# Performance work log

Measured on AMD Instinct MI355X. Metric: run time of the kernel, lower is better.

## Reference

```python
import jax, jax.numpy as jnp
import numpy as np

N, K, B, C, H = 12000, 32, 1, 64, 64
ALPHA = 0.3  # keras LeakyReLU default

def leaky(x):
    return jnp.where(x >= 0, x, ALPHA * x)

def setup_inputs() -> dict:
    key = jax.random.key(0)
    ks = jax.random.split(key, 8)
    def dense_init(k, fan_in, fan_out):
        lim = np.sqrt(6.0 / (fan_in + fan_out))
        return jax.random.uniform(k, (fan_in, fan_out), jnp.float32, -lim, lim)
    return {
        "embeddings": jax.random.normal(ks[0], (B, N, C), jnp.float32),
        "weights": jax.random.uniform(ks[1], (N, N), jnp.float32),
        "neighbor_set": jax.random.randint(ks[2], (N, K), 0, N, jnp.int64) if jax.config.jax_enable_x64 else jax.random.randint(ks[2], (N, K), 0, N, jnp.int32),
        "Q0_w": dense_init(ks[3], C, H), "Q0_b": jnp.zeros((H,), jnp.float32),
        "W0_w": dense_init(ks[4], C + H, H), "W0_b": jnp.zeros((H,), jnp.float32),
        "Q1_w": dense_init(ks[5], H, H), "Q1_b": jnp.zeros((H,), jnp.float32),
        "W1_w": dense_init(ks[6], H + H, H), "W1_b": jnp.zeros((H,), jnp.float32),
    }

def convolve(emb, weights, nbr, Qw, Qb, Ww, Wb):
    # emb: [B,N,C], weights: [N,N], nbr: [N,K]
    nb_emb = emb[:, nbr, :]                       # [B,N,K,C] gather neighbors
    nb_hid = leaky(jnp.einsum('bnkc,ch->bnkh', nb_emb, Qw) + Qb)  # [B,N,K,H]
    nb_w = weights[jnp.arange(nbr.shape[0])[:, None], nbr]        # [N,K]
    nb_w = nb_w[None, :, :, None]                                  # [1,N,K,1]
    agg = jnp.sum(nb_hid * nb_w, axis=2) / (jnp.sum(nb_w, axis=2) + 1e-6)  # [B,N,H]
    cat = jnp.concatenate([emb, agg], axis=-1)     # [B,N,C+H]
    out = leaky(jnp.einsum('bnd,dh->bnh', cat, Ww) + Wb)
    return out / (jnp.linalg.norm(out, axis=2, keepdims=True) + 1e-6)

def reference(embeddings, weights, neighbor_set, Q0_w, Q0_b, W0_w, W0_b, Q1_w, Q1_b, W1_w, W1_b):
    x = convolve(embeddings, weights, neighbor_set, Q0_w, Q0_b, W0_w, W0_b)
    x = convolve(x, weights, neighbor_set, Q1_w, Q1_b, W1_w, W1_b)
    return x
```

## Files before the change

kernel.cpp:

```cpp
#include <hip/hip_runtime.h>
#include <math.h>

#define ALPHA 0.3f
#define KN 32

__device__ __forceinline__ float leaky_f(float x) { return x >= 0.f ? x : ALPHA * x; }

__global__ __launch_bounds__(256) void k_dense_gather(
    const float* __restrict__ X,
    const float* __restrict__ Qw,
    const float* __restrict__ Qb,
    const float* __restrict__ wmat,
    const int*  __restrict__ nbr,
    float* __restrict__ wcache,
    float* __restrict__ Hout,
    int N)
{
    __shared__ float sQ[64 * 64];
    __shared__ float sX[4][64];
    const int tid  = threadIdx.x;
    const int wid  = tid >> 6;
    const int lane = tid & 63;
    const int bs   = blockIdx.x * 16;

    int gid[2]; float gw[2];
    #pragma unroll
    for (int u = 0; u < 2; ++u) {
        int e = tid + u * 256;
        int n = bs + (e >> 5); if (n >= N) n = N - 1;
        gid[u] = nbr[(size_t)n * KN + (e & 31)];
    }
    #pragma unroll
    for (int u = 0; u < 2; ++u) {
        int e = tid + u * 256;
        int n = bs + (e >> 5); if (n >= N) n = N - 1;
        gw[u] = wmat[(size_t)n * (size_t)N + gid[u]];
    }

    {
        const float4* s = (const float4*)Qw; float4* d = (float4*)sQ;
        #pragma unroll
        for (int i = 0; i < 4; ++i) d[i * 256 + tid] = s[i * 256 + tid];
    }
    __syncthreads();

    const float qb = Qb[lane];
    #pragma unroll
    for (int g = 0; g < 4; ++g) {
        int nr = bs + g * 4 + wid;
        int n  = nr < N ? nr : N - 1;
        sX[wid][lane] = X[(size_t)n * 64 + lane];
        float acc = qb;
        #pragma unroll
        for (int c = 0; c < 64; ++c)
            acc = fmaf(sX[wid][c], sQ[c * 64 + lane], acc);
        if (nr < N) Hout[(size_t)n * 64 + lane] = leaky_f(acc);
    }

    if (wcache) {
        #pragma unroll
        for (int u = 0; u < 2; ++u) {
            int e = tid + u * 256;
            if (bs + (e >> 5) < N) wcache[(size_t)bs * KN + e] = gw[u];
        }
    }
}

template<bool FUSE>
__global__ __launch_bounds__(256) void k_conv(
    const float* __restrict__ X,
    const float* __restrict__ Hbuf,
    const float* __restrict__ Wmat,
    const float* __restrict__ wcache,
    const int*  __restrict__ nbr,
    const float* __restrict__ Ww,
    const float* __restrict__ Wb,
    const float* __restrict__ Q1w,
    const float* __restrict__ Q1b,
    float* __restrict__ OUT,
    float* __restrict__ H1out,
    int N, int mode)
{
    __shared__ float sW[128 * 64];
    __shared__ float sw[4][32];
    __shared__ int   snb[4][32];
    __shared__ float sx[4][64];
    __shared__ float sa[4][64];

    const int tid  = threadIdx.x;
    const int wid  = tid >> 6;
    const int lane = tid & 63;
    const int bs   = blockIdx.x * 8;

    int n0 = bs + wid; if (n0 >= N) n0 = N - 1;
    float x0 = X[(size_t)n0 * 64 + lane];
    int id0 = 0; float wv0 = 0.f;
    if (lane < KN) {
        id0 = nbr[(size_t)n0 * KN + lane];
        wv0 = (mode == 1) ? wcache[(size_t)n0 * KN + lane]
                          : Wmat[(size_t)n0 * (size_t)N + id0];
    }

    {
        const float4* s = (const float4*)Ww; float4* d = (float4*)sW;
        #pragma unroll
        for (int i = 0; i < 8; ++i) d[i * 256 + tid] = s[i * 256 + tid];
    }
    sx[wid][lane] = x0;
    if (lane < KN) { snb[wid][lane] = id0; sw[wid][lane] = wv0; }
    __syncthreads();

    const float wb = Wb[lane];
    const float qb = FUSE ? Q1b[lane] : 0.f;

    float x1 = 0.f; int id1 = 0; float wv1 = 0.f;

    #pragma unroll
    for (int g = 0; g < 2; ++g) {
        const int nr = bs + g * 4 + wid;

        if (g == 0) {
            int n1 = bs + 4 + wid; if (n1 >= N) n1 = N - 1;
            x1 = X[(size_t)n1 * 64 + lane];
            if (lane < KN) {
                id1 = nbr[(size_t)n1 * KN + lane];
                wv1 = (mode == 1) ? wcache[(size_t)n1 * KN + lane]
                                  : Wmat[(size_t)n1 * (size_t)N + id1];
            }
        }

        float sumw = 0.f;
        #pragma unroll
        for (int k = 0; k < KN; ++k) sumw += sw[wid][k];

        float agg = 0.f;
        #pragma unroll 8
        for (int k = 0; k < KN; ++k) {
            size_t id = (size_t)snb[wid][k];
            agg = fmaf(sw[wid][k], Hbuf[id * 64 + lane], agg);
        }
        sa[wid][lane] = agg / (sumw + 1e-6f);

        float acc = wb;
        #pragma unroll
        for (int c = 0; c < 64; ++c)
            acc = fmaf(sx[wid][c], sW[c * 64 + lane], acc);
        #pragma unroll
        for (int c = 0; c < 64; ++c)
            acc = fmaf(sa[wid][c], sW[(64 + c) * 64 + lane], acc);

        float o = leaky_f(acc);
        float ss = o * o;
        #pragma unroll
        for (int off = 32; off; off >>= 1) ss += __shfl_xor(ss, off);
        const float on = o / (sqrtf(ss) + 1e-6f);
        if (nr < N) OUT[(size_t)nr * 64 + lane] = on;

        if (FUSE) {
            float acc1 = qb;
            #pragma unroll 8
            for (int c = 0; c < 64; ++c)
                acc1 = fmaf(__shfl(on, c), Q1w[c * 64 + lane], acc1);
            if (nr < N) H1out[(size_t)nr * 64 + lane] = leaky_f(acc1);
        }

        if (g == 0) {
            sx[wid][lane] = x1;
            if (lane < KN) { snb[wid][lane] = id1; sw[wid][lane] = wv1; }
        }
    }
}

extern "C" void kernel_launch(void* const* d_in, const int* in_sizes, int n_in,
                              void* d_out, int out_size, void* d_ws, size_t ws_size,
                              hipStream_t stream)
{
    const float* emb  = (const float*)d_in[0];
    const float* wmat = (const float*)d_in[1];
    const int*   nbr  = (const int*)  d_in[2];
    const float* Q0w  = (const float*)d_in[3];
    const float* Q0b  = (const float*)d_in[4];
    const float* W0w  = (const float*)d_in[5];
    const float* W0b  = (const float*)d_in[6];
    const float* Q1w  = (const float*)d_in[7];
    const float* Q1b  = (const float*)d_in[8];
    const float* W1w  = (const float*)d_in[9];
    const float* W1b  = (const float*)d_in[10];
    float* out = (float*)d_out;

    const int N = in_sizes[2] / KN;
    const size_t hbuf_bytes = (size_t)N * 64 * sizeof(float);
    const size_t wc_bytes   = (size_t)N * KN * sizeof(float);

    float* h0 = (float*)d_ws;
    float* h1 = (float*)((char*)d_ws + hbuf_bytes);
    bool use_wc = ws_size >= 2 * hbuf_bytes + wc_bytes;
    float* wcache = use_wc ? (float*)((char*)d_ws + 2 * hbuf_bytes) : nullptr;
    const int mode = use_wc ? 1 : 0;

    const int gridA = (N + 15) / 16;
    const int gridC = (N + 7) / 8;

    k_dense_gather<<<gridA, 256, 0, stream>>>(emb, Q0w, Q0b, wmat, nbr,
                                              wcache, h0, N);
    k_conv<true><<<gridC, 256, 0, stream>>>(emb, h0, wmat, wcache, nbr,
                                            W0w, W0b, Q1w, Q1b, out, h1, N, mode);
    k_conv<false><<<gridC, 256, 0, stream>>>(out, h1, wmat, wcache, nbr,
                                             W1w, W1b, nullptr, nullptr,
                                             out, nullptr, N, mode);
}
```

Before: 64.06 us.

## Transpose and swizzle weight tiles in LDS, process two nodes per wavefront

Weight matrices are stored transposed in shared memory with an XOR swizzle, so each lane reads float4 rows of its own output column and the input vectors are read as float4 broadcasts. Each wavefront now computes two nodes at once, reusing every weight load across both. The neighbour-gather loops for the two nodes are interleaved, with neighbour ids and weights passed by shuffle instead of LDS. The gather now runs before the weight-staging barrier rather than after it. The gains come from fewer LDS instructions and more memory-level parallelism, at the cost of higher register use and a more scattered LDS write pattern during staging.

```diff
diff --git a/kernel.cpp b/kernel.cpp
--- a/kernel.cpp
+++ b/kernel.cpp
@@ -16,8 +16,9 @@
     float* __restrict__ Hout,
     int N)
 {
-    __shared__ float sQ[64 * 64];
-    __shared__ float sX[4][64];
+    __shared__ float4 sQT[64][16];
+    __shared__ float  sX[4][2][64];
+
     const int tid  = threadIdx.x;
     const int wid  = tid >> 6;
     const int lane = tid & 63;
@@ -38,23 +39,47 @@
     }
 
     {
-        const float4* s = (const float4*)Qw; float4* d = (float4*)sQ;
-        #pragma unroll
-        for (int i = 0; i < 4; ++i) d[i * 256 + tid] = s[i * 256 + tid];
+        const float4* s = (const float4*)Qw;
+        #pragma unroll
+        for (int i = 0; i < 4; ++i) {
+            int idx = i * 256 + tid;
+            float4 v = s[idx];
+            int c  = idx >> 4;
+            int h4 = idx & 15;
+            #pragma unroll
+            for (int u = 0; u < 4; ++u) {
+                int h = h4 * 4 + u;
+                ((float*)&sQT[h][(c >> 2) ^ (h & 7)])[c & 3] = (&v.x)[u];
+            }
+        }
     }
     __syncthreads();
 
     const float qb = Qb[lane];
     #pragma unroll
-    for (int g = 0; g < 4; ++g) {
-        int nr = bs + g * 4 + wid;
-        int n  = nr < N ? nr : N - 1;
-        sX[wid][lane] = X[(size_t)n * 64 + lane];
-        float acc = qb;
-        #pragma unroll
-        for (int c = 0; c < 64; ++c)
-            acc = fmaf(sX[wid][c], sQ[c * 64 + lane], acc);
-        if (nr < N) Hout[(size_t)n * 64 + lane] = leaky_f(acc);
+    for (int p = 0; p < 2; ++p) {
+        int n0 = bs + p * 8 + wid * 2;
+        int n1 = n0 + 1;
+        int m0 = n0 < N ? n0 : N - 1;
+        int m1 = n1 < N ? n1 : N - 1;
+        sX[wid][0][lane] = X[(size_t)m0 * 64 + lane];
+        sX[wid][1][lane] = X[(size_t)m1 * 64 + lane];
+        const float4* x40 = (const float4*)sX[wid][0];
+        const float4* x41 = (const float4*)sX[wid][1];
+
+        float a0 = qb, a1 = qb;
+        #pragma unroll
+        for (int c4 = 0; c4 < 16; ++c4) {
+            float4 wv = sQT[lane][c4 ^ (lane & 7)];
+            float4 v0 = x40[c4], v1 = x41[c4];
+            #pragma unroll
+            for (int u = 0; u < 4; ++u) {
+                a0 = fmaf((&v0.x)[u], (&wv.x)[u], a0);
+                a1 = fmaf((&v1.x)[u], (&wv.x)[u], a1);
+            }
+        }
+        if (n0 < N) Hout[(size_t)n0 * 64 + lane] = leaky_f(a0);
+        if (n1 < N) Hout[(size_t)n1 * 64 + lane] = leaky_f(a1);
     }
 
     if (wcache) {
@@ -81,93 +106,116 @@
     float* __restrict__ H1out,
     int N, int mode)
 {
-    __shared__ float sW[128 * 64];
-    __shared__ float sw[4][32];
-    __shared__ int   snb[4][32];
-    __shared__ float sx[4][64];
-    __shared__ float sa[4][64];
+    __shared__ float4 sWT[64][32];
+    __shared__ float  sx[4][2][64];
+    __shared__ float  sa[4][2][64];
 
     const int tid  = threadIdx.x;
     const int wid  = tid >> 6;
     const int lane = tid & 63;
     const int bs   = blockIdx.x * 8;
 
-    int n0 = bs + wid; if (n0 >= N) n0 = N - 1;
-    float x0 = X[(size_t)n0 * 64 + lane];
-    int id0 = 0; float wv0 = 0.f;
-    if (lane < KN) {
-        id0 = nbr[(size_t)n0 * KN + lane];
-        wv0 = (mode == 1) ? wcache[(size_t)n0 * KN + lane]
-                          : Wmat[(size_t)n0 * (size_t)N + id0];
-    }
+    const int na = bs + wid * 2;
+    const int nb = na + 1;
+    const int ma = na < N ? na : N - 1;
+    const int mb = nb < N ? nb : N - 1;
+
+    const int  myn = (lane < 32) ? ma : mb;
+    const int  myk = lane & 31;
+    const int  id  = nbr[(size_t)myn * KN + myk];
+    const float w  = (mode == 1) ? wcache[(size_t)myn * KN + myk]
+                                 : Wmat[(size_t)myn * (size_t)N + id];
+    float xa = X[(size_t)ma * 64 + lane];
+    float xb = X[(size_t)mb * 64 + lane];
 
     {
-        const float4* s = (const float4*)Ww; float4* d = (float4*)sW;
-        #pragma unroll
-        for (int i = 0; i < 8; ++i) d[i * 256 + tid] = s[i * 256 + tid];
-    }
-    sx[wid][lane] = x0;
-    if (lane < KN) { snb[wid][lane] = id0; sw[wid][lane] = wv0; }
+        const float4* s = (const float4*)Ww;
+        #pragma unroll
+        for (int i = 0; i < 8; ++i) {
+            int idx = i * 256 + tid;
+            float4 v = s[idx];
+            int c  = idx >> 4;
+            int h4 = idx & 15;
+            #pragma unroll
+            for (int u = 0; u < 4; ++u) {
+                int h = h4 * 4 + u;
+                ((float*)&sWT[h][(c >> 2) ^ (h & 7)])[c & 3] = (&v.x)[u];
+            }
+        }
+    }
+    sx[wid][0][lane] = xa;
+    sx[wid][1][lane] = xb;
+
+    float s32 = w;
+    #pragma unroll
+    for (int off = 16; off; off >>= 1) s32 += __shfl_xor(s32, off);
+    const float sumwa = __shfl(s32, 0);
+    const float sumwb = __shfl(s32, 32);
+
+    float agga = 0.f, aggb = 0.f;
+    #pragma unroll 8
+    for (int k = 0; k < KN; ++k) {
+        int   ia = __shfl(id, k);
+        float wa = __shfl(w,  k);
+        int   ib = __shfl(id, 32 + k);
+        float wv = __shfl(w,  32 + k);
+        agga = fmaf(wa, Hbuf[(size_t)ia * 64 + lane], agga);
+        aggb = fmaf(wv, Hbuf[(size_t)ib * 64 + lane], aggb);
+    }
+    sa[wid][0][lane] = agga / (sumwa + 1e-6f);
+    sa[wid][1][lane] = aggb / (sumwb + 1e-6f);
     __syncthreads();
 
+    const float4* x4a = (const float4*)sx[wid][0];
+    const float4* x4b = (const float4*)sx[wid][1];
+    const float4* a4a = (const float4*)sa[wid][0];
+    const float4* a4b = (const float4*)sa[wid][1];
+
     const float wb = Wb[lane];
-    const float qb = FUSE ? Q1b[lane] : 0.f;
-
-    float x1 = 0.f; int id1 = 0; float wv1 = 0.f;
-
-    #pragma unroll
-    for (int g = 0; g < 2; ++g) {
-        const int nr = bs + g * 4 + wid;
-
-        if (g == 0) {
-            int n1 = bs + 4 + wid; if (n1 >= N) n1 = N - 1;
-            x1 = X[(size_t)n1 * 64 + lane];
-            if (lane < KN) {
-                id1 = nbr[(size_t)n1 * KN + lane];
-                wv1 = (mode == 1) ? wcache[(size_t)n1 * KN + lane]
-                                  : Wmat[(size_t)n1 * (size_t)N + id1];
-            }
-        }
-
-        float sumw = 0.f;
-        #pragma unroll
-        for (int k = 0; k < KN; ++k) sumw += sw[wid][k];
-
-        float agg = 0.f;
+    float acca = wb, accb = wb;
+    #pragma unroll
+    for (int c4 = 0; c4 < 16; ++c4) {
+        float4 wv = sWT[lane][c4 ^ (lane & 7)];
+        float4 va = x4a[c4], vb = x4b[c4];
+        #pragma unroll
+        for (int u = 0; u < 4; ++u) {
+            acca = fmaf((&va.x)[u], (&wv.x)[u], acca);
+            accb = fmaf((&vb.x)[u], (&wv.x)[u], accb);
+        }
+    }
+    #pragma unroll
+    for (int c4 = 0; c4 < 16; ++c4) {
+        float4 wv = sWT[lane][(16 + c4) ^ (lane & 7)];
+        float4 va = a4a[c4], vb = a4b[c4];
+        #pragma unroll
+        for (int u = 0; u < 4; ++u) {
+            acca = fmaf((&va.x)[u], (&wv.x)[u], acca);
+            accb = fmaf((&vb.x)[u], (&wv.x)[u], accb);
+        }
+    }
+
+    float oa = leaky_f(acca), ob = leaky_f(accb);
+    float ssa = oa * oa, ssb = ob * ob;
+    #pragma unroll
+    for (int off = 32; off; off >>= 1) {
+        ssa += __shfl_xor(ssa, off);
+        ssb += __shfl_xor(ssb, off);
+    }
+    const float ona = oa / (sqrtf(ssa) + 1e-6f);
+    const float onb = ob / (sqrtf(ssb) + 1e-6f);
+    if (na < N) OUT[(size_t)na * 64 + lane] = ona;
+    if (nb < N) OUT[(size_t)nb * 64 + lane] = onb;
+
+    if (FUSE) {
+        float acc1a = Q1b[lane], acc1b = acc1a;
         #pragma unroll 8
-        for (int k = 0; k < KN; ++k) {
-            size_t id = (size_t)snb[wid][k];
-            agg = fmaf(sw[wid][k], Hbuf[id * 64 + lane], agg);
-        }
-        sa[wid][lane] = agg / (sumw + 1e-6f);
-
-        float acc = wb;
-        #pragma unroll
-        for (int c = 0; c < 64; ++c)
-            acc = fmaf(sx[wid][c], sW[c * 64 + lane], acc);
-        #pragma unroll
-        for (int c = 0; c < 64; ++c)
-            acc = fmaf(sa[wid][c], sW[(64 + c) * 64 + lane], acc);
-
-        float o = leaky_f(acc);
-        float ss = o * o;
-        #pragma unroll
-        for (int off = 32; off; off >>= 1) ss += __shfl_xor(ss, off);
-        const float on = o / (sqrtf(ss) + 1e-6f);
-        if (nr < N) OUT[(size_t)nr * 64 + lane] = on;
-
-        if (FUSE) {
-            float acc1 = qb;
-            #pragma unroll 8
-            for (int c = 0; c < 64; ++c)
-                acc1 = fmaf(__shfl(on, c), Q1w[c * 64 + lane], acc1);
-            if (nr < N) H1out[(size_t)nr * 64 + lane] = leaky_f(acc1);
-        }
-
-        if (g == 0) {
-            sx[wid][lane] = x1;
-            if (lane < KN) { snb[wid][lane] = id1; sw[wid][lane] = wv1; }
-        }
+        for (int c = 0; c < 64; ++c) {
+            float q = Q1w[c * 64 + lane];
+            acc1a = fmaf(__shfl(ona, c), q, acc1a);
+            acc1b = fmaf(__shfl(onb, c), q, acc1b);
+        }
+        if (na < N) H1out[(size_t)na * 64 + lane] = leaky_f(acc1a);
+        if (nb < N) H1out[(size_t)nb * 64 + lane] = leaky_f(acc1b);
     }
 }
 
```

After: 75.84 us. 18.4% more time.
